# Optimization experiments

Hardware: AMD Instinct MI355X
Metric: run time of the kernel (lower is better)

## Reference

```python
import jax, jax.numpy as jnp
import numpy as np

N = 400_000
E = 3_200_000
K = 5
H = 100
F_IN = 2
L = 5
BN_EPS = 1e-5


def setup_inputs() -> dict:
    key = jax.random.key(0)
    ks = jax.random.split(key, 6)
    x = jax.random.normal(ks[0], (N, F_IN), dtype=jnp.float32)
    edge_index = jax.random.randint(ks[1], (2, E), 0, N, dtype=jnp.int64)
    W0 = jax.random.normal(ks[2], (K, F_IN, H), dtype=jnp.float32) * 0.1
    b0 = jnp.zeros((H,), dtype=jnp.float32)
    Wr = jax.random.normal(ks[3], (L - 1, K, H, H), dtype=jnp.float32) * 0.1
    br = jnp.zeros((L - 1, H), dtype=jnp.float32)
    gamma = jnp.ones((L, H), dtype=jnp.float32)
    beta = jnp.zeros((L, H), dtype=jnp.float32)
    return {"x": x, "edge_index": edge_index, "W0": W0, "b0": b0,
            "Wr": Wr, "br": br, "gamma": gamma, "beta": beta}


def reference(x, edge_index, W0, b0, Wr, br, gamma, beta):
    n = x.shape[0]
    src, dst = edge_index[0], edge_index[1]

    # ChebConv normalization (lambda_max = 2, sym): L_hat = -D^{-1/2} A D^{-1/2}
    deg = jax.ops.segment_sum(jnp.ones(src.shape, jnp.float32), src, num_segments=n)
    dinv = jnp.where(deg > 0, jax.lax.rsqrt(jnp.maximum(deg, 1.0)), 0.0)
    norm = -dinv[src] * dinv[dst]  # [E]

    def prop(h):
        # out[i] = sum_{(j->i)} norm_e * h[j]
        return jax.ops.segment_sum(norm[:, None] * h[src], dst, num_segments=n)

    def cheb(h, W, b):
        # Chebyshev recurrence: T0 = h, T1 = L_hat h, Tk = 2 L_hat T_{k-1} - T_{k-2}
        Tx0 = h
        out = Tx0 @ W[0] + b
        Tx1 = prop(Tx0)
        out = out + Tx1 @ W[1]
        for k in range(2, W.shape[0]):
            Tx2 = 2.0 * prop(Tx1) - Tx0
            out = out + Tx2 @ W[k]
            Tx0, Tx1 = Tx1, Tx2
        return out

    def batch_norm(h, g, bt):
        m = h.mean(axis=0)
        v = h.var(axis=0)  # biased, as torch BN uses for normalization
        return g * (h - m) * jax.lax.rsqrt(v + BN_EPS) + bt

    h = x
    for layer in range(L):
        W = W0 if layer == 0 else Wr[layer - 1]
        b = b0 if layer == 0 else br[layer - 1]
        h = batch_norm(jax.nn.relu(cheb(h, W, b)), gamma[layer], beta[layer])
    return h
```

## Files before the change

### kernel.cpp

```cpp
#include <hip/hip_runtime.h>

#define H 100
#define FIN 2
#define KORD 5
#define NPB 64
#define SE_CAP 2048

typedef unsigned int uint32;
typedef unsigned short ushort16;
typedef __attribute__((ext_vector_type(8))) short s8v;
typedef __attribute__((ext_vector_type(4))) float f4v;

__device__ __forceinline__ ushort16 f2b(float x) {
  uint32 u = __float_as_uint(x);
  return (ushort16)((u + 0x7fffu + ((u >> 16) & 1u)) >> 16);
}
__device__ __forceinline__ float2 b2f2(uint32 v) {
  return make_float2(__uint_as_float(v << 16), __uint_as_float(v & 0xffff0000u));
}
__device__ __forceinline__ void acc8(float* a, uint4 v, float w) {
  float2 f;
  f = b2f2(v.x); a[0] = fmaf(w, f.x, a[0]); a[1] = fmaf(w, f.y, a[1]);
  f = b2f2(v.y); a[2] = fmaf(w, f.x, a[2]); a[3] = fmaf(w, f.y, a[3]);
  f = b2f2(v.z); a[4] = fmaf(w, f.x, a[4]); a[5] = fmaf(w, f.y, a[5]);
  f = b2f2(v.w); a[6] = fmaf(w, f.x, a[6]); a[7] = fmaf(w, f.y, a[7]);
}


__global__ __launch_bounds__(256) void deg_kernel(const int* __restrict__ src, const int* __restrict__ dst,
                                                  float* __restrict__ deg, int* __restrict__ indeg, int E) {
  int e = blockIdx.x * 256 + threadIdx.x;
  if (e < E) {
    atomicAdd(&deg[src[e]], 1.0f);
    atomicAdd(&indeg[dst[e]], 1);
  }
}

__global__ __launch_bounds__(256) void dinv_kernel(const float* __restrict__ deg, float* __restrict__ dinv, int n) {
  int i = blockIdx.x * 256 + threadIdx.x;
  if (i < n) {
    float d = deg[i];
    dinv[i] = d > 0.f ? rsqrtf(fmaxf(d, 1.f)) : 0.f;
  }
}

__global__ __launch_bounds__(256) void scan_block(const int* __restrict__ in, int* __restrict__ incl,
                                                  int* __restrict__ bsum, int n) {
  __shared__ int s[256];
  int i = blockIdx.x * 256 + threadIdx.x;
  int v = (i < n) ? in[i] : 0;
  s[threadIdx.x] = v;
  __syncthreads();
  for (int d = 1; d < 256; d <<= 1) {
    int t = (threadIdx.x >= d) ? s[threadIdx.x - d] : 0;
    __syncthreads();
    s[threadIdx.x] += t;
    __syncthreads();
  }
  if (i < n) incl[i] = s[threadIdx.x];
  if (threadIdx.x == 255) bsum[blockIdx.x] = s[255];
}

__global__ __launch_bounds__(256) void scan_sums(const int* __restrict__ bsum, int* __restrict__ bscan, int nb) {
  __shared__ int s[256];
  __shared__ int carry;
  if (threadIdx.x == 0) carry = 0;
  __syncthreads();
  for (int base = 0; base < nb; base += 256) {
    int i = base + threadIdx.x;
    int v = (i < nb) ? bsum[i] : 0;
    s[threadIdx.x] = v;
    __syncthreads();
    for (int d = 1; d < 256; d <<= 1) {
      int t = (threadIdx.x >= d) ? s[threadIdx.x - d] : 0;
      __syncthreads();
      s[threadIdx.x] += t;
      __syncthreads();
    }
    int c = carry;
    if (i < nb) bscan[i] = s[threadIdx.x] + c;
    __syncthreads();
    if (threadIdx.x == 0) carry = c + s[255];
    __syncthreads();
  }
}

__global__ __launch_bounds__(256) void finalize_offsets(const int* __restrict__ incl, const int* __restrict__ indeg,
                                                        const int* __restrict__ bscan, int* __restrict__ offsets,
                                                        int* __restrict__ cursor, int n, int total) {
  int i = blockIdx.x * 256 + threadIdx.x;
  if (i < n) {
    int prev = (blockIdx.x > 0) ? bscan[blockIdx.x - 1] : 0;
    int excl = incl[i] - indeg[i] + prev;
    offsets[i] = excl;
    cursor[i] = excl;
  }
  if (i == 0) offsets[n] = total;
}

__global__ __launch_bounds__(256) void build_csr(const int* __restrict__ src, const int* __restrict__ dst,
                                                 const float* __restrict__ dinv, int* __restrict__ cursor,
                                                 int2* __restrict__ csr, int E) {
  int e = blockIdx.x * 256 + threadIdx.x;
  if (e < E) {
    int s = src[e], d = dst[e];
    float nrm = -dinv[s] * dinv[d];
    int p = atomicAdd(&cursor[d], 1);
    csr[p] = make_int2(s, __float_as_int(nrm));
  }
}

__global__ __launch_bounds__(256) void pad_zero(uint4* __restrict__ b, int nrows) {
  int i = blockIdx.x * 256 + threadIdx.x;
  if (i < nrows * 4) {
    uint4 z; z.x = 0; z.y = 0; z.z = 0; z.w = 0;
    b[(size_t)(i >> 2) * 16 + 12 + (i & 3)] = z;
  }
}


__global__ __launch_bounds__(256) void prop2(const float* __restrict__ h, const float* __restrict__ prev,
                                             float* __restrict__ out, const int* __restrict__ offs,
                                             const int2* __restrict__ csr, int n, int mode) {
  int i = blockIdx.x * 256 + threadIdx.x;
  if (i >= n) return;
  float a0 = 0.f, a1 = 0.f;
  int e0 = offs[i], e1 = offs[i + 1];
  int e = e0;
  for (; e + 4 <= e1; e += 4) {
    int2 c0 = csr[e], c1 = csr[e + 1], c2 = csr[e + 2], c3 = csr[e + 3];
    float w0 = __int_as_float(c0.y), w1 = __int_as_float(c1.y);
    float w2 = __int_as_float(c2.y), w3 = __int_as_float(c3.y);
    float x0 = h[2 * c0.x], y0 = h[2 * c0.x + 1];
    float x1 = h[2 * c1.x], y1 = h[2 * c1.x + 1];
    float x2 = h[2 * c2.x], y2 = h[2 * c2.x + 1];
    float x3 = h[2 * c3.x], y3 = h[2 * c3.x + 1];
    a0 = fmaf(w0, x0, a0); a1 = fmaf(w0, y0, a1);
    a0 = fmaf(w1, x1, a0); a1 = fmaf(w1, y1, a1);
    a0 = fmaf(w2, x2, a0); a1 = fmaf(w2, y2, a1);
    a0 = fmaf(w3, x3, a0); a1 = fmaf(w3, y3, a1);
  }
  for (; e < e1; ++e) {
    int2 c = csr[e];
    float w = __int_as_float(c.y);
    a0 = fmaf(w, h[2 * c.x], a0);
    a1 = fmaf(w, h[2 * c.x + 1], a1);
  }
  if (mode) {
    a0 = 2.f * a0 - prev[2 * i];
    a1 = 2.f * a1 - prev[2 * i + 1];
  }
  out[2 * i] = a0;
  out[2 * i + 1] = a1;
}

__global__ __launch_bounds__(256) void prop_hb3(const uint32* __restrict__ h, const uint32* __restrict__ prev,
                                                uint32* __restrict__ out, const int* __restrict__ offs,
                                                const int2* __restrict__ csr, int n, int mode) {
  __shared__ int2 se[SE_CAP];
  __shared__ int soff[NPB + 1];
  int t = threadIdx.x;
  int n0 = blockIdx.x * NPB;
  if (t <= NPB) {
    int idx = n0 + t;
    soff[t] = offs[idx < n ? idx : n];
  }
  __syncthreads();
  int e0b = soff[0], e1b = soff[NPB];
  bool staged = (e1b - e0b) <= SE_CAP;
  if (staged) {
    for (int i = e0b + t; i < e1b; i += 256) se[i - e0b] = csr[i];
  }
  __syncthreads();

  int w = t >> 6, lane = t & 63, grp = lane >> 4, sub = lane & 15;
  const uint4* hq = (const uint4*)h;
  uint4* oq = (uint4*)out;
  bool wr = (grp == 0);
  int base = w * 16;
  int cnt = 16;
  if (n0 + base + 16 > n) cnt = n - (n0 + base);
  if (cnt <= 0) return;

  auto nrOf = [&](int li) {
    int d = soff[base + li + 1] - soff[base + li];
    int r = (d + 7) >> 3;
    return r ? r : 1;
  };
  auto issueLoads = [&](int li, int r, uint4& v0, uint4& v1, float& w0, float& w1) {
    int e0 = soff[base + li];
    int deg = soff[base + li + 1] - e0;
    int ea = 8 * r + grp;
    int2 ca = make_int2(0, 0), cb = make_int2(0, 0);
    if (staged) {
      int eb = e0 - e0b;
      if (ea < deg) ca = se[eb + ea];
      if (ea + 4 < deg) cb = se[eb + ea + 4];
    } else {
      if (ea < deg) ca = csr[e0 + ea];
      if (ea + 4 < deg) cb = csr[e0 + ea + 4];
    }
    v0 = hq[(size_t)ca.x * 16 + sub];
    v1 = hq[(size_t)cb.x * 16 + sub];
    w0 = __int_as_float(ca.y);
    w1 = __int_as_float(cb.y);
  };
  auto finishNode = [&](int li, float* a) {
    int node = n0 + base + li;
    size_t qi = (size_t)node * 16 + sub;
    uint4 pv; pv.x = 0; pv.y = 0; pv.z = 0; pv.w = 0;
    if (mode && wr && sub < 13) pv = ((const uint4*)prev)[qi];
#pragma unroll
    for (int j = 0; j < 8; ++j) a[j] += __shfl_xor(a[j], 16);
#pragma unroll
    for (int j = 0; j < 8; ++j) a[j] += __shfl_xor(a[j], 32);
    if (!wr) return;
    if (sub >= 13) {
      uint4 z; z.x = 0; z.y = 0; z.z = 0; z.w = 0;
      oq[qi] = z;
      return;
    }
    if (sub == 12) { a[4] = 0.f; a[5] = 0.f; a[6] = 0.f; a[7] = 0.f; }
    float rr[8];
    if (mode) {
      float2 p;
      p = b2f2(pv.x); rr[0] = 2.f * a[0] - p.x; rr[1] = 2.f * a[1] - p.y;
      p = b2f2(pv.y); rr[2] = 2.f * a[2] - p.x; rr[3] = 2.f * a[3] - p.y;
      p = b2f2(pv.z); rr[4] = 2.f * a[4] - p.x; rr[5] = 2.f * a[5] - p.y;
      p = b2f2(pv.w); rr[6] = 2.f * a[6] - p.x; rr[7] = 2.f * a[7] - p.y;
    } else {
#pragma unroll
      for (int j = 0; j < 8; ++j) rr[j] = a[j];
    }
    uint4 pk;
    pk.x = (uint32)f2b(rr[0]) | ((uint32)f2b(rr[1]) << 16);
    pk.y = (uint32)f2b(rr[2]) | ((uint32)f2b(rr[3]) << 16);
    pk.z = (uint32)f2b(rr[4]) | ((uint32)f2b(rr[5]) << 16);
    pk.w = (uint32)f2b(rr[6]) | ((uint32)f2b(rr[7]) << 16);
    oq[qi] = pk;
  };

  float a[8];
#pragma unroll
  for (int j = 0; j < 8; ++j) a[j] = 0.f;
  int li = 0, r = 0, nr = nrOf(0);
  uint4 va, vb;
  float wa, wb;
  issueLoads(0, 0, va, vb, wa, wb);
  for (;;) {
    int nli = li, nrr = r + 1;
    bool fin = (nrr >= nr);
    if (fin) { nli = li + 1; nrr = 0; }
    bool more = (nli < cnt);
    uint4 va2, vb2;
    float wa2 = 0.f, wb2 = 0.f;
    if (more) issueLoads(nli, nrr, va2, vb2, wa2, wb2);
    acc8(a, va, wa);
    acc8(a, vb, wb);
    if (fin) {
      finishNode(li, a);
#pragma unroll
      for (int j = 0; j < 8; ++j) a[j] = 0.f;
      if (more) nr = nrOf(nli);
    }
    if (!more) break;
    li = nli; r = nrr;
    va = va2; vb = vb2; wa = wa2; wb = wb2;
  }
}


__global__ __launch_bounds__(64) void wconv(const float* __restrict__ Wr, ushort16* __restrict__ Wf) {
  int b = blockIdx.x;
  int l = threadIdx.x;
  int mat = b / 28, rem = b % 28;
  int kc = rem / 7, ft = rem % 7;
  const float* Wm = Wr + (size_t)mat * H * H;
  int c0 = kc * 32 + (l >> 4) * 8;
  int f = ft * 16 + (l & 15);
  ushort16 vals[8];
#pragma unroll
  for (int j = 0; j < 8; ++j) {
    int c = c0 + j;
    float v = (c < H && f < H) ? Wm[c * H + f] : 0.f;
    vals[j] = f2b(v);
  }
  uint4 pk;
  pk.x = (uint32)vals[0] | ((uint32)vals[1] << 16);
  pk.y = (uint32)vals[2] | ((uint32)vals[3] << 16);
  pk.z = (uint32)vals[4] | ((uint32)vals[5] << 16);
  pk.w = (uint32)vals[6] | ((uint32)vals[7] << 16);
  *(uint4*)(Wf + (size_t)b * 512 + l * 8) = pk;
}


__global__ __launch_bounds__(256) void gemm_mfma(const ushort16* __restrict__ Ta, const ushort16* __restrict__ Tb,
                                                 const ushort16* __restrict__ Tc, const ushort16* __restrict__ Td,
                                                 const ushort16* __restrict__ Te, int nk,
                                                 const ushort16* __restrict__ Wf, const float* __restrict__ bias,
                                                 float* __restrict__ C, int n, int initMode,
                                                 float* __restrict__ stats, int doStats) {
  __shared__ float sred[4][2][112];
  int t = threadIdx.x;
  int w = t >> 6, l = t & 63;
  int ml = l & 15, quad = l >> 4;
  int n0 = blockIdx.x * 128 + 32 * w;

  f4v acc[2][7];
  if (initMode) {
#pragma unroll
    for (int ft = 0; ft < 7; ++ft) {
      int f = ft * 16 + ml;
      float b = (f < H) ? bias[f] : 0.f;
      f4v v = {b, b, b, b};
      acc[0][ft] = v;
      acc[1][ft] = v;
    }
  } else {
#pragma unroll
    for (int s = 0; s < 2; ++s)
#pragma unroll
      for (int ft = 0; ft < 7; ++ft) {
        int f = ft * 16 + ml;
#pragma unroll
        for (int r = 0; r < 4; ++r) {
          int row = n0 + 16 * s + quad * 4 + r;
          acc[s][ft][r] = (f < H && row < n) ? C[(size_t)row * H + f] : 0.f;
        }
      }
  }

  for (int k = 0; k < nk; ++k) {
    const ushort16* T = (k == 0) ? Ta : (k == 1) ? Tb : (k == 2) ? Tc : (k == 3) ? Td : Te;
#pragma unroll
    for (int kc = 0; kc < 4; ++kc) {
      s8v bfrag[7];
      const ushort16* wb = Wf + ((size_t)(k * 4 + kc) * 7) * 512 + l * 8;
#pragma unroll
      for (int ft = 0; ft < 7; ++ft) bfrag[ft] = *(const s8v*)(wb + ft * 512);
#pragma unroll
      for (int s = 0; s < 2; ++s) {
        const ushort16* ap = T + (size_t)(n0 + 16 * s + ml) * 128 + kc * 32 + quad * 8;
        s8v a = *(const s8v*)ap;
#pragma unroll
        for (int ft = 0; ft < 7; ++ft)
          acc[s][ft] = __builtin_amdgcn_mfma_f32_16x16x32_bf16(a, bfrag[ft], acc[s][ft], 0, 0, 0);
      }
    }
  }

#pragma unroll
  for (int s = 0; s < 2; ++s)
#pragma unroll
    for (int ft = 0; ft < 7; ++ft) {
      int f = ft * 16 + ml;
      if (f < H) {
#pragma unroll
        for (int r = 0; r < 4; ++r) {
          int row = n0 + 16 * s + quad * 4 + r;
          if (row < n) C[(size_t)row * H + f] = acc[s][ft][r];
        }
      }
    }

  if (doStats) {
#pragma unroll
    for (int ft = 0; ft < 7; ++ft) {
      float s1 = 0.f, s2 = 0.f;
#pragma unroll
      for (int s = 0; s < 2; ++s)
#pragma unroll
        for (int r = 0; r < 4; ++r) {
          int row = n0 + 16 * s + quad * 4 + r;
          float v = (row < n) ? fmaxf(acc[s][ft][r], 0.f) : 0.f;
          s1 += v;
          s2 = fmaf(v, v, s2);
        }
      s1 += __shfl_xor(s1, 16); s1 += __shfl_xor(s1, 32);
      s2 += __shfl_xor(s2, 16); s2 += __shfl_xor(s2, 32);
      if (quad == 0) {
        sred[w][0][ft * 16 + ml] = s1;
        sred[w][1][ft * 16 + ml] = s2;
      }
    }
    __syncthreads();
    if (t < 112 && t < H) {
      float s1 = sred[0][0][t] + sred[1][0][t] + sred[2][0][t] + sred[3][0][t];
      float s2 = sred[0][1][t] + sred[1][1][t] + sred[2][1][t] + sred[3][1][t];
      atomicAdd(&stats[t], s1);
      atomicAdd(&stats[128 + t], s2);
    }
  }
}


__global__ __launch_bounds__(128) void layer0_out(const float* __restrict__ x, const float* __restrict__ t1,
                                                  const float* __restrict__ t2, const float* __restrict__ t3,
                                                  const float* __restrict__ t4, const float* __restrict__ W0,
                                                  const float* __restrict__ b0, float* __restrict__ C, int n) {
  int f = threadIdx.x;
  bool act = f < H;
  float w[10];
  float b = 0.f;
  if (act) {
#pragma unroll
    for (int j = 0; j < 10; ++j) w[j] = W0[j * H + f];
    b = b0[f];
  }
  int n0 = blockIdx.x * 32;
  int n1 = n0 + 32 < n ? n0 + 32 : n;
  for (int i = n0; i < n1; ++i) {
    if (!act) continue;
    float acc = b;
    acc = fmaf(x[2 * i],      w[0], acc);
    acc = fmaf(x[2 * i + 1],  w[1], acc);
    acc = fmaf(t1[2 * i],     w[2], acc);
    acc = fmaf(t1[2 * i + 1], w[3], acc);
    acc = fmaf(t2[2 * i],     w[4], acc);
    acc = fmaf(t2[2 * i + 1], w[5], acc);
    acc = fmaf(t3[2 * i],     w[6], acc);
    acc = fmaf(t3[2 * i + 1], w[7], acc);
    acc = fmaf(t4[2 * i],     w[8], acc);
    acc = fmaf(t4[2 * i + 1], w[9], acc);
    C[(size_t)i * H + f] = acc;
  }
}


__global__ __launch_bounds__(128) void bn_stats(const float* __restrict__ acc, float* __restrict__ stats, int n) {
  int f = threadIdx.x;
  int n0 = blockIdx.x * 512;
  int n1 = n0 + 512 < n ? n0 + 512 : n;
  if (f < H) {
    float s = 0.f, s2 = 0.f;
    for (int i = n0; i < n1; ++i) {
      float v = fmaxf(acc[(size_t)i * H + f], 0.f);
      s += v;
      s2 = fmaf(v, v, s2);
    }
    atomicAdd(&stats[f], s);
    atomicAdd(&stats[128 + f], s2);
  }
}

__global__ __launch_bounds__(128) void bn_params(float* __restrict__ stats, const float* __restrict__ gamma,
                                                 const float* __restrict__ beta, int n) {
  int f = threadIdx.x;
  if (f >= H) return;
  float inv_n = 1.f / (float)n;
  float m = stats[f] * inv_n;
  float v = stats[128 + f] * inv_n - m * m;
  float is = rsqrtf(v + 1e-5f);
  float g = gamma[f] * is;
  stats[256 + f] = g;
  stats[384 + f] = beta[f] - m * g;
}

__global__ __launch_bounds__(256) void bn_final(const float* __restrict__ acc, const float* __restrict__ mi,
                                                float* __restrict__ out, int total) {
  int idx = blockIdx.x * 256 + threadIdx.x;
  if (idx >= total) return;
  int f = idx % H;
  float v = fmaxf(acc[idx], 0.f);
  out[idx] = fmaf(v, mi[f], mi[128 + f]);
}

__global__ __launch_bounds__(256) void bn_final_bf16v(const float* __restrict__ acc, const float* __restrict__ mi,
                                                      uint4* __restrict__ out, int n) {
  int idx = blockIdx.x * 256 + threadIdx.x;
  if (idx >= n * 13) return;
  int row = idx / 13, s = idx - row * 13;
  int f0 = s * 8;
  const float* cr = acc + (size_t)row * H;
  float v[8];
#pragma unroll
  for (int j = 0; j < 8; ++j) {
    int f = f0 + j;
    int fc = (f < H) ? f : 0;
    float c = fmaxf(cr[fc], 0.f);
    v[j] = (f < H) ? fmaf(c, mi[f], mi[128 + f]) : 0.f;
  }
  uint4 pk;
  pk.x = (uint32)f2b(v[0]) | ((uint32)f2b(v[1]) << 16);
  pk.y = (uint32)f2b(v[2]) | ((uint32)f2b(v[3]) << 16);
  pk.z = (uint32)f2b(v[4]) | ((uint32)f2b(v[5]) << 16);
  pk.w = (uint32)f2b(v[6]) | ((uint32)f2b(v[7]) << 16);
  out[(size_t)row * 16 + s] = pk;
}


extern "C" void kernel_launch(void* const* d_in, const int* in_sizes, int n_in,
                              void* d_out, int out_size, void* d_ws, size_t ws_size,
                              hipStream_t stream) {
  const float* x     = (const float*)d_in[0];
  const int*   ei    = (const int*)d_in[1];
  const float* W0    = (const float*)d_in[2];
  const float* b0    = (const float*)d_in[3];
  const float* Wr    = (const float*)d_in[4];
  const float* br    = (const float*)d_in[5];
  const float* gamma = (const float*)d_in[6];
  const float* beta  = (const float*)d_in[7];
  float* C = (float*)d_out;

  const int N = in_sizes[0] / FIN;
  const int E = in_sizes[1] / 2;
  const int* src = ei;
  const int* dst = ei + E;

  char* ws = (char*)d_ws;
  size_t off = 0;
  auto alloc = [&](size_t bytes) -> void* {
    void* p = ws + off;
    off = (off + bytes + 255) & ~(size_t)255;
    return p;
  };

  size_t TB = (size_t)N * 128 * sizeof(ushort16);
  ushort16* B0     = (ushort16*)alloc(TB);
  ushort16* B1     = (ushort16*)alloc(TB);
  ushort16* B2     = (ushort16*)alloc(TB);
  ushort16* Wf     = (ushort16*)alloc((size_t)20 * 14336 * sizeof(ushort16));
  float* t1       = (float*)alloc((size_t)N * 2 * 4);
  float* t2       = (float*)alloc((size_t)N * 2 * 4);
  float* t3       = (float*)alloc((size_t)N * 2 * 4);
  float* t4       = (float*)alloc((size_t)N * 2 * 4);
  float* deg      = (float*)alloc((size_t)N * 4);
  int*   indeg    = (int*)alloc((size_t)N * 4);
  float* dinv     = (float*)alloc((size_t)N * 4);
  int*   incl     = (int*)alloc((size_t)N * 4);
  int*   bsum     = (int*)alloc(8192 * 4);
  int*   bscan    = (int*)alloc(8192 * 4);
  int*   offsets  = (int*)alloc((size_t)(N + 1) * 4);
  int*   cursor   = (int*)alloc((size_t)N * 4);
  int2*  csr      = (int2*)alloc((size_t)E * 8);
  float* stats    = (float*)alloc(512 * 4);

  ushort16* B3 = B0;
  ushort16* B4 = B1;
  bool five = (off + 2 * TB + 512 <= ws_size);
  if (five) {
    B3 = (ushort16*)alloc(TB);
    B4 = (ushort16*)alloc(TB);
  }

  int gE = (E + 255) / 256;
  int gN = (N + 255) / 256;

  hipMemsetAsync(deg, 0, (size_t)N * 4, stream);
  hipMemsetAsync(indeg, 0, (size_t)N * 4, stream);

  deg_kernel<<<gE, 256, 0, stream>>>(src, dst, deg, indeg, E);
  dinv_kernel<<<gN, 256, 0, stream>>>(deg, dinv, N);
  scan_block<<<gN, 256, 0, stream>>>(indeg, incl, bsum, N);
  scan_sums<<<1, 256, 0, stream>>>(bsum, bscan, gN);
  finalize_offsets<<<gN, 256, 0, stream>>>(incl, indeg, bscan, offsets, cursor, N, E);
  build_csr<<<gE, 256, 0, stream>>>(src, dst, dinv, cursor, csr, E);
  wconv<<<20 * 28, 64, 0, stream>>>(Wr, Wf);
  pad_zero<<<(N * 4 + 255) / 256, 256, 0, stream>>>((uint4*)B0, N);

  prop2<<<gN, 256, 0, stream>>>(x,  x,  t1, offsets, csr, N, 0);
  prop2<<<gN, 256, 0, stream>>>(t1, x,  t2, offsets, csr, N, 1);
  prop2<<<gN, 256, 0, stream>>>(t2, t1, t3, offsets, csr, N, 1);
  prop2<<<gN, 256, 0, stream>>>(t3, t2, t4, offsets, csr, N, 1);
  layer0_out<<<(N + 31) / 32, 128, 0, stream>>>(x, t1, t2, t3, t4, W0, b0, C, N);
  hipMemsetAsync(stats, 0, 1024, stream);
  bn_stats<<<(N + 511) / 512, 128, 0, stream>>>(C, stats, N);
  bn_params<<<1, 128, 0, stream>>>(stats, gamma, beta, N);
  bn_final_bf16v<<<(N * 13 + 255) / 256, 256, 0, stream>>>(C, stats + 256, (uint4*)B0, N);

  int gG = (N + 127) / 128;
  int gP = (N + NPB - 1) / NPB;
  for (int layer = 1; layer < 5; ++layer) {
    const ushort16* WfL = Wf + (size_t)(layer - 1) * 5 * 14336;
    const float* bl = br + (size_t)(layer - 1) * H;
    if (five) {
      prop_hb3<<<gP, 256, 0, stream>>>((const uint32*)B0, (const uint32*)B0, (uint32*)B1, offsets, csr, N, 0);
      prop_hb3<<<gP, 256, 0, stream>>>((const uint32*)B1, (const uint32*)B0, (uint32*)B2, offsets, csr, N, 1);
      prop_hb3<<<gP, 256, 0, stream>>>((const uint32*)B2, (const uint32*)B1, (uint32*)B3, offsets, csr, N, 1);
      prop_hb3<<<gP, 256, 0, stream>>>((const uint32*)B3, (const uint32*)B2, (uint32*)B4, offsets, csr, N, 1);
      hipMemsetAsync(stats, 0, 1024, stream);
      gemm_mfma<<<gG, 256, 0, stream>>>(B0, B1, B2, B3, B4, 5, WfL, bl, C, N, 1, stats, 1);
    } else {
      prop_hb3<<<gP, 256, 0, stream>>>((const uint32*)B0, (const uint32*)B0, (uint32*)B1, offsets, csr, N, 0);
      prop_hb3<<<gP, 256, 0, stream>>>((const uint32*)B1, (const uint32*)B0, (uint32*)B2, offsets, csr, N, 1);
      gemm_mfma<<<gG, 256, 0, stream>>>(B0, B1, B2, B0, B1, 3, WfL, bl, C, N, 1, stats, 0);
      prop_hb3<<<gP, 256, 0, stream>>>((const uint32*)B2, (const uint32*)B1, (uint32*)B0, offsets, csr, N, 1);
      prop_hb3<<<gP, 256, 0, stream>>>((const uint32*)B0, (const uint32*)B2, (uint32*)B1, offsets, csr, N, 1);
      gemm_mfma<<<gG, 256, 0, stream>>>(B0, B1, B0, B0, B1, 2, WfL + (size_t)3 * 14336, bl, C, N, 0, stats, 0);
      hipMemsetAsync(stats, 0, 1024, stream);
      bn_stats<<<(N + 511) / 512, 128, 0, stream>>>(C, stats, N);
    }
    bn_params<<<1, 128, 0, stream>>>(stats, gamma + (size_t)layer * H, beta + (size_t)layer * H, N);
    if (layer < 4)
      bn_final_bf16v<<<(N * 13 + 255) / 256, 256, 0, stream>>>(C, stats + 256, (uint4*)B0, N);
    else
      bn_final<<<(N * H + 255) / 256, 256, 0, stream>>>(C, stats + 256, C, N * H);
  }
}
```

Baseline: 4.915 ms.

## Split bf16 feature buffers into 96-wide main and 4-wide tail arrays

Measured after the change: 5.239 ms. +6.6%, slower.

```diff
diff --git a/kernel.cpp b/kernel.cpp
--- a/kernel.cpp
+++ b/kernel.cpp
@@ -107,14 +107,6 @@
     float nrm = -dinv[s] * dinv[d];
     int p = atomicAdd(&cursor[d], 1);
     csr[p] = make_int2(s, __float_as_int(nrm));
-  }
-}
-
-__global__ __launch_bounds__(256) void pad_zero(uint4* __restrict__ b, int nrows) {
-  int i = blockIdx.x * 256 + threadIdx.x;
-  if (i < nrows * 4) {
-    uint4 z; z.x = 0; z.y = 0; z.z = 0; z.w = 0;
-    b[(size_t)(i >> 2) * 16 + 12 + (i & 3)] = z;
   }
 }
 
@@ -154,9 +146,11 @@
   out[2 * i + 1] = a1;
 }
 
-__global__ __launch_bounds__(256) void prop_hb3(const uint32* __restrict__ h, const uint32* __restrict__ prev,
-                                                uint32* __restrict__ out, const int* __restrict__ offs,
-                                                const int2* __restrict__ csr, int n, int mode) {
+__global__ __launch_bounds__(256) void prop_hs(const uint4* __restrict__ mIn, const uint2* __restrict__ tIn,
+                                               const uint4* __restrict__ mPrev, const uint2* __restrict__ tPrev,
+                                               uint4* __restrict__ mOut, uint2* __restrict__ tOut,
+                                               const int* __restrict__ offs, const int2* __restrict__ csr,
+                                               int n, int mode) {
   __shared__ int2 se[SE_CAP];
   __shared__ int soff[NPB + 1];
   int t = threadIdx.x;
@@ -174,8 +168,6 @@
   __syncthreads();
 
   int w = t >> 6, lane = t & 63, grp = lane >> 4, sub = lane & 15;
-  const uint4* hq = (const uint4*)h;
-  uint4* oq = (uint4*)out;
   bool wr = (grp == 0);
   int base = w * 16;
   int cnt = 16;
@@ -200,27 +192,31 @@
       if (ea < deg) ca = csr[e0 + ea];
       if (ea + 4 < deg) cb = csr[e0 + ea + 4];
     }
-    v0 = hq[(size_t)ca.x * 16 + sub];
-    v1 = hq[(size_t)cb.x * 16 + sub];
+    uint4 z; z.x = 0; z.y = 0; z.z = 0; z.w = 0;
+    v0 = z; v1 = z;
+    if (sub < 12) {
+      v0 = mIn[(size_t)ca.x * 12 + sub];
+      v1 = mIn[(size_t)cb.x * 12 + sub];
+    } else if (sub == 12) {
+      uint2 ta = tIn[ca.x], tb = tIn[cb.x];
+      v0.x = ta.x; v0.y = ta.y;
+      v1.x = tb.x; v1.y = tb.y;
+    }
     w0 = __int_as_float(ca.y);
     w1 = __int_as_float(cb.y);
   };
   auto finishNode = [&](int li, float* a) {
     int node = n0 + base + li;
-    size_t qi = (size_t)node * 16 + sub;
     uint4 pv; pv.x = 0; pv.y = 0; pv.z = 0; pv.w = 0;
-    if (mode && wr && sub < 13) pv = ((const uint4*)prev)[qi];
+    if (mode && wr) {
+      if (sub < 12) pv = mPrev[(size_t)node * 12 + sub];
+      else if (sub == 12) { uint2 tp = tPrev[node]; pv.x = tp.x; pv.y = tp.y; }
+    }
 #pragma unroll
     for (int j = 0; j < 8; ++j) a[j] += __shfl_xor(a[j], 16);
 #pragma unroll
     for (int j = 0; j < 8; ++j) a[j] += __shfl_xor(a[j], 32);
-    if (!wr) return;
-    if (sub >= 13) {
-      uint4 z; z.x = 0; z.y = 0; z.z = 0; z.w = 0;
-      oq[qi] = z;
-      return;
-    }
-    if (sub == 12) { a[4] = 0.f; a[5] = 0.f; a[6] = 0.f; a[7] = 0.f; }
+    if (!wr || sub > 12) return;
     float rr[8];
     if (mode) {
       float2 p;
@@ -232,12 +228,19 @@
 #pragma unroll
       for (int j = 0; j < 8; ++j) rr[j] = a[j];
     }
-    uint4 pk;
-    pk.x = (uint32)f2b(rr[0]) | ((uint32)f2b(rr[1]) << 16);
-    pk.y = (uint32)f2b(rr[2]) | ((uint32)f2b(rr[3]) << 16);
-    pk.z = (uint32)f2b(rr[4]) | ((uint32)f2b(rr[5]) << 16);
-    pk.w = (uint32)f2b(rr[6]) | ((uint32)f2b(rr[7]) << 16);
-    oq[qi] = pk;
+    if (sub < 12) {
+      uint4 pk;
+      pk.x = (uint32)f2b(rr[0]) | ((uint32)f2b(rr[1]) << 16);
+      pk.y = (uint32)f2b(rr[2]) | ((uint32)f2b(rr[3]) << 16);
+      pk.z = (uint32)f2b(rr[4]) | ((uint32)f2b(rr[5]) << 16);
+      pk.w = (uint32)f2b(rr[6]) | ((uint32)f2b(rr[7]) << 16);
+      mOut[(size_t)node * 12 + sub] = pk;
+    } else {
+      uint2 pk;
+      pk.x = (uint32)f2b(rr[0]) | ((uint32)f2b(rr[1]) << 16);
+      pk.y = (uint32)f2b(rr[2]) | ((uint32)f2b(rr[3]) << 16);
+      tOut[node] = pk;
+    }
   };
 
   float a[8];
@@ -294,44 +297,33 @@
 }
 
 
-__global__ __launch_bounds__(256) void gemm_mfma(const ushort16* __restrict__ Ta, const ushort16* __restrict__ Tb,
-                                                 const ushort16* __restrict__ Tc, const ushort16* __restrict__ Td,
-                                                 const ushort16* __restrict__ Te, int nk,
+__global__ __launch_bounds__(256) void gemm_mfma(const ushort16* __restrict__ m0, const uint2* __restrict__ t0,
+                                                 const ushort16* __restrict__ m1, const uint2* __restrict__ t1,
+                                                 const ushort16* __restrict__ m2, const uint2* __restrict__ t2,
+                                                 const ushort16* __restrict__ m3, const uint2* __restrict__ t3,
+                                                 const ushort16* __restrict__ m4, const uint2* __restrict__ t4,
                                                  const ushort16* __restrict__ Wf, const float* __restrict__ bias,
-                                                 float* __restrict__ C, int n, int initMode,
-                                                 float* __restrict__ stats, int doStats) {
+                                                 float* __restrict__ C, int n, float* __restrict__ stats) {
   __shared__ float sred[4][2][112];
-  int t = threadIdx.x;
-  int w = t >> 6, l = t & 63;
+  int tid = threadIdx.x;
+  int w = tid >> 6, l = tid & 63;
   int ml = l & 15, quad = l >> 4;
   int n0 = blockIdx.x * 128 + 32 * w;
 
   f4v acc[2][7];
-  if (initMode) {
-#pragma unroll
-    for (int ft = 0; ft < 7; ++ft) {
-      int f = ft * 16 + ml;
-      float b = (f < H) ? bias[f] : 0.f;
-      f4v v = {b, b, b, b};
-      acc[0][ft] = v;
-      acc[1][ft] = v;
-    }
-  } else {
-#pragma unroll
-    for (int s = 0; s < 2; ++s)
-#pragma unroll
-      for (int ft = 0; ft < 7; ++ft) {
-        int f = ft * 16 + ml;
-#pragma unroll
-        for (int r = 0; r < 4; ++r) {
-          int row = n0 + 16 * s + quad * 4 + r;
-          acc[s][ft][r] = (f < H && row < n) ? C[(size_t)row * H + f] : 0.f;
-        }
-      }
-  }
-
-  for (int k = 0; k < nk; ++k) {
-    const ushort16* T = (k == 0) ? Ta : (k == 1) ? Tb : (k == 2) ? Tc : (k == 3) ? Td : Te;
+#pragma unroll
+  for (int ft = 0; ft < 7; ++ft) {
+    int f = ft * 16 + ml;
+    float b = (f < H) ? bias[f] : 0.f;
+    f4v v = {b, b, b, b};
+    acc[0][ft] = v;
+    acc[1][ft] = v;
+  }
+
+#pragma unroll
+  for (int k = 0; k < 5; ++k) {
+    const ushort16* Tm = (k == 0) ? m0 : (k == 1) ? m1 : (k == 2) ? m2 : (k == 3) ? m3 : m4;
+    const uint2* Tt = (k == 0) ? t0 : (k == 1) ? t1 : (k == 2) ? t2 : (k == 3) ? t3 : t4;
 #pragma unroll
     for (int kc = 0; kc < 4; ++kc) {
       s8v bfrag[7];
@@ -340,8 +332,19 @@
       for (int ft = 0; ft < 7; ++ft) bfrag[ft] = *(const s8v*)(wb + ft * 512);
 #pragma unroll
       for (int s = 0; s < 2; ++s) {
-        const ushort16* ap = T + (size_t)(n0 + 16 * s + ml) * 128 + kc * 32 + quad * 8;
-        s8v a = *(const s8v*)ap;
+        int row = n0 + 16 * s + ml;
+        s8v a;
+        if (kc < 3) {
+          a = *(const s8v*)(Tm + (size_t)row * 96 + kc * 32 + quad * 8);
+        } else {
+          s8v az = {0, 0, 0, 0, 0, 0, 0, 0};
+          if (quad == 0) {
+            uint2 tv = Tt[row];
+            az[0] = (short)(tv.x & 0xffffu); az[1] = (short)(tv.x >> 16);
+            az[2] = (short)(tv.y & 0xffffu); az[3] = (short)(tv.y >> 16);
+          }
+          a = az;
+        }
 #pragma unroll
         for (int ft = 0; ft < 7; ++ft)
           acc[s][ft] = __builtin_amdgcn_mfma_f32_16x16x32_bf16(a, bfrag[ft], acc[s][ft], 0, 0, 0);
@@ -363,33 +366,31 @@
       }
     }
 
-  if (doStats) {
-#pragma unroll
-    for (int ft = 0; ft < 7; ++ft) {
-      float s1 = 0.f, s2 = 0.f;
-#pragma unroll
-      for (int s = 0; s < 2; ++s)
-#pragma unroll
-        for (int r = 0; r < 4; ++r) {
-          int row = n0 + 16 * s + quad * 4 + r;
-          float v = (row < n) ? fmaxf(acc[s][ft][r], 0.f) : 0.f;
-          s1 += v;
-          s2 = fmaf(v, v, s2);
-        }
-      s1 += __shfl_xor(s1, 16); s1 += __shfl_xor(s1, 32);
-      s2 += __shfl_xor(s2, 16); s2 += __shfl_xor(s2, 32);
-      if (quad == 0) {
-        sred[w][0][ft * 16 + ml] = s1;
-        sred[w][1][ft * 16 + ml] = s2;
+#pragma unroll
+  for (int ft = 0; ft < 7; ++ft) {
+    float s1 = 0.f, s2 = 0.f;
+#pragma unroll
+    for (int s = 0; s < 2; ++s)
+#pragma unroll
+      for (int r = 0; r < 4; ++r) {
+        int row = n0 + 16 * s + quad * 4 + r;
+        float v = (row < n) ? fmaxf(acc[s][ft][r], 0.f) : 0.f;
+        s1 += v;
+        s2 = fmaf(v, v, s2);
       }
-    }
-    __syncthreads();
-    if (t < 112 && t < H) {
-      float s1 = sred[0][0][t] + sred[1][0][t] + sred[2][0][t] + sred[3][0][t];
-      float s2 = sred[0][1][t] + sred[1][1][t] + sred[2][1][t] + sred[3][1][t];
-      atomicAdd(&stats[t], s1);
-      atomicAdd(&stats[128 + t], s2);
-    }
+    s1 += __shfl_xor(s1, 16); s1 += __shfl_xor(s1, 32);
+    s2 += __shfl_xor(s2, 16); s2 += __shfl_xor(s2, 32);
+    if (quad == 0) {
+      sred[w][0][ft * 16 + ml] = s1;
+      sred[w][1][ft * 16 + ml] = s2;
+    }
+  }
+  __syncthreads();
+  if (tid < H) {
+    float s1 = sred[0][0][tid] + sred[1][0][tid] + sred[2][0][tid] + sred[3][0][tid];
+    float s2 = sred[0][1][tid] + sred[1][1][tid] + sred[2][1][tid] + sred[3][1][tid];
+    atomicAdd(&stats[tid], s1);
+    atomicAdd(&stats[128 + tid], s2);
   }
 }
 
@@ -465,27 +466,40 @@
   out[idx] = fmaf(v, mi[f], mi[128 + f]);
 }
 
-__global__ __launch_bounds__(256) void bn_final_bf16v(const float* __restrict__ acc, const float* __restrict__ mi,
-                                                      uint4* __restrict__ out, int n) {
+__global__ __launch_bounds__(256) void bn_final_split(const float* __restrict__ acc, const float* __restrict__ mi,
+                                                      uint4* __restrict__ mOut, uint2* __restrict__ tOut, int n) {
   int idx = blockIdx.x * 256 + threadIdx.x;
   if (idx >= n * 13) return;
   int row = idx / 13, s = idx - row * 13;
-  int f0 = s * 8;
   const float* cr = acc + (size_t)row * H;
-  float v[8];
-#pragma unroll
-  for (int j = 0; j < 8; ++j) {
-    int f = f0 + j;
-    int fc = (f < H) ? f : 0;
-    float c = fmaxf(cr[fc], 0.f);
-    v[j] = (f < H) ? fmaf(c, mi[f], mi[128 + f]) : 0.f;
-  }
-  uint4 pk;
-  pk.x = (uint32)f2b(v[0]) | ((uint32)f2b(v[1]) << 16);
-  pk.y = (uint32)f2b(v[2]) | ((uint32)f2b(v[3]) << 16);
-  pk.z = (uint32)f2b(v[4]) | ((uint32)f2b(v[5]) << 16);
-  pk.w = (uint32)f2b(v[6]) | ((uint32)f2b(v[7]) << 16);
-  out[(size_t)row * 16 + s] = pk;
+  if (s < 12) {
+    int f0 = s * 8;
+    float v[8];
+#pragma unroll
+    for (int j = 0; j < 8; ++j) {
+      int f = f0 + j;
+      float c = fmaxf(cr[f], 0.f);
+      v[j] = fmaf(c, mi[f], mi[128 + f]);
+    }
+    uint4 pk;
+    pk.x = (uint32)f2b(v[0]) | ((uint32)f2b(v[1]) << 16);
+    pk.y = (uint32)f2b(v[2]) | ((uint32)f2b(v[3]) << 16);
+    pk.z = (uint32)f2b(v[4]) | ((uint32)f2b(v[5]) << 16);
+    pk.w = (uint32)f2b(v[6]) | ((uint32)f2b(v[7]) << 16);
+    mOut[(size_t)row * 12 + s] = pk;
+  } else {
+    float v[4];
+#pragma unroll
+    for (int j = 0; j < 4; ++j) {
+      int f = 96 + j;
+      float c = fmaxf(cr[f], 0.f);
+      v[j] = fmaf(c, mi[f], mi[128 + f]);
+    }
+    uint2 pk;
+    pk.x = (uint32)f2b(v[0]) | ((uint32)f2b(v[1]) << 16);
+    pk.y = (uint32)f2b(v[2]) | ((uint32)f2b(v[3]) << 16);
+    tOut[row] = pk;
+  }
 }
 
 
@@ -515,33 +529,27 @@
     return p;
   };
 
-  size_t TB = (size_t)N * 128 * sizeof(ushort16);
-  ushort16* B0     = (ushort16*)alloc(TB);
-  ushort16* B1     = (ushort16*)alloc(TB);
-  ushort16* B2     = (ushort16*)alloc(TB);
-  ushort16* Wf     = (ushort16*)alloc((size_t)20 * 14336 * sizeof(ushort16));
-  float* t1       = (float*)alloc((size_t)N * 2 * 4);
-  float* t2       = (float*)alloc((size_t)N * 2 * 4);
-  float* t3       = (float*)alloc((size_t)N * 2 * 4);
-  float* t4       = (float*)alloc((size_t)N * 2 * 4);
-  float* deg      = (float*)alloc((size_t)N * 4);
-  int*   indeg    = (int*)alloc((size_t)N * 4);
-  float* dinv     = (float*)alloc((size_t)N * 4);
-  int*   incl     = (int*)alloc((size_t)N * 4);
-  int*   bsum     = (int*)alloc(8192 * 4);
-  int*   bscan    = (int*)alloc(8192 * 4);
-  int*   offsets  = (int*)alloc((size_t)(N + 1) * 4);
-  int*   cursor   = (int*)alloc((size_t)N * 4);
-  int2*  csr      = (int2*)alloc((size_t)E * 8);
-  float* stats    = (float*)alloc(512 * 4);
-
-  ushort16* B3 = B0;
-  ushort16* B4 = B1;
-  bool five = (off + 2 * TB + 512 <= ws_size);
-  if (five) {
-    B3 = (ushort16*)alloc(TB);
-    B4 = (ushort16*)alloc(TB);
-  }
+  size_t MBsz = (size_t)N * 96 * 2;
+  size_t TBsz = (size_t)N * 8;
+  ushort16* Bm[5];
+  uint2*    Bt[5];
+  for (int i = 0; i < 5; ++i) Bm[i] = (ushort16*)alloc(MBsz);
+  for (int i = 0; i < 5; ++i) Bt[i] = (uint2*)alloc(TBsz);
+  ushort16* Wf   = (ushort16*)alloc((size_t)20 * 14336 * sizeof(ushort16));
+  float* t1      = (float*)alloc((size_t)N * 2 * 4);
+  float* t2      = (float*)alloc((size_t)N * 2 * 4);
+  float* t3      = (float*)alloc((size_t)N * 2 * 4);
+  float* t4      = (float*)alloc((size_t)N * 2 * 4);
+  float* deg     = (float*)alloc((size_t)N * 4);
+  int*   indeg   = (int*)alloc((size_t)N * 4);
+  float* dinv    = (float*)alloc((size_t)N * 4);
+  int*   incl    = (int*)alloc((size_t)N * 4);
+  int*   bsum    = (int*)alloc(8192 * 4);
+  int*   bscan   = (int*)alloc(8192 * 4);
+  int*   offsets = (int*)alloc((size_t)(N + 1) * 4);
+  int*   cursor  = (int*)alloc((size_t)N * 4);
+  int2*  csr     = (int2*)alloc((size_t)E * 8);
+  float* stats   = (float*)alloc(512 * 4);
 
   int gE = (E + 255) / 256;
   int gN = (N + 255) / 256;
@@ -556,7 +564,6 @@
   finalize_offsets<<<gN, 256, 0, stream>>>(incl, indeg, bscan, offsets, cursor, N, E);
   build_csr<<<gE, 256, 0, stream>>>(src, dst, dinv, cursor, csr, E);
   wconv<<<20 * 28, 64, 0, stream>>>(Wr, Wf);
-  pad_zero<<<(N * 4 + 255) / 256, 256, 0, stream>>>((uint4*)B0, N);
 
   prop2<<<gN, 256, 0, stream>>>(x,  x,  t1, offsets, csr, N, 0);
   prop2<<<gN, 256, 0, stream>>>(t1, x,  t2, offsets, csr, N, 1);
@@ -566,33 +573,27 @@
   hipMemsetAsync(stats, 0, 1024, stream);
   bn_stats<<<(N + 511) / 512, 128, 0, stream>>>(C, stats, N);
   bn_params<<<1, 128, 0, stream>>>(stats, gamma, beta, N);
-  bn_final_bf16v<<<(N * 13 + 255) / 256, 256, 0, stream>>>(C, stats + 256, (uint4*)B0, N);
+  bn_final_split<<<(N * 13 + 255) / 256, 256, 0, stream>>>(C, stats + 256, (uint4*)Bm[0], Bt[0], N);
 
   int gG = (N + 127) / 128;
   int gP = (N + NPB - 1) / NPB;
   for (int layer = 1; layer < 5; ++layer) {
     const ushort16* WfL = Wf + (size_t)(layer - 1) * 5 * 14336;
     const float* bl = br + (size_t)(layer - 1) * H;
-    if (five) {
-      prop_hb3<<<gP, 256, 0, stream>>>((const uint32*)B0, (const uint32*)B0, (uint32*)B1, offsets, csr, N, 0);
-      prop_hb3<<<gP, 256, 0, stream>>>((const uint32*)B1, (const uint32*)B0, (uint32*)B2, offsets, csr, N, 1);
-      prop_hb3<<<gP, 256, 0, stream>>>((const uint32*)B2, (const uint32*)B1, (uint32*)B3, offsets, csr, N, 1);
-      prop_hb3<<<gP, 256, 0, stream>>>((const uint32*)B3, (const uint32*)B2, (uint32*)B4, offsets, csr, N, 1);
-      hipMemsetAsync(stats, 0, 1024, stream);
-      gemm_mfma<<<gG, 256, 0, stream>>>(B0, B1, B2, B3, B4, 5, WfL, bl, C, N, 1, stats, 1);
-    } else {
-      prop_hb3<<<gP, 256, 0, stream>>>((const uint32*)B0, (const uint32*)B0, (uint32*)B1, offsets, csr, N, 0);
-      prop_hb3<<<gP, 256, 0, stream>>>((const uint32*)B1, (const uint32*)B0, (uint32*)B2, offsets, csr, N, 1);
-      gemm_mfma<<<gG, 256, 0, stream>>>(B0, B1, B2, B0, B1, 3, WfL, bl, C, N, 1, stats, 0);
-      prop_hb3<<<gP, 256, 0, stream>>>((const uint32*)B2, (const uint32*)B1, (uint32*)B0, offsets, csr, N, 1);
-      prop_hb3<<<gP, 256, 0, stream>>>((const uint32*)B0, (const uint32*)B2, (uint32*)B1, offsets, csr, N, 1);
-      gemm_mfma<<<gG, 256, 0, stream>>>(B0, B1, B0, B0, B1, 2, WfL + (size_t)3 * 14336, bl, C, N, 0, stats, 0);
-      hipMemsetAsync(stats, 0, 1024, stream);
-      bn_stats<<<(N + 511) / 512, 128, 0, stream>>>(C, stats, N);
-    }
+    prop_hs<<<gP, 256, 0, stream>>>((const uint4*)Bm[0], Bt[0], (const uint4*)Bm[0], Bt[0],
+                                    (uint4*)Bm[1], Bt[1], offsets, csr, N, 0);
+    prop_hs<<<gP, 256, 0, stream>>>((const uint4*)Bm[1], Bt[1], (const uint4*)Bm[0], Bt[0],
+                                    (uint4*)Bm[2], Bt[2], offsets, csr, N, 1);
+    prop_hs<<<gP, 256, 0, stream>>>((const uint4*)Bm[2], Bt[2], (const uint4*)Bm[1], Bt[1],
+                                    (uint4*)Bm[3], Bt[3], offsets, csr, N, 1);
+    prop_hs<<<gP, 256, 0, stream>>>((const uint4*)Bm[3], Bt[3], (const uint4*)Bm[2], Bt[2],
+                                    (uint4*)Bm[4], Bt[4], offsets, csr, N, 1);
+    hipMemsetAsync(stats, 0, 1024, stream);
+    gemm_mfma<<<gG, 256, 0, stream>>>(Bm[0], Bt[0], Bm[1], Bt[1], Bm[2], Bt[2], Bm[3], Bt[3], Bm[4], Bt[4],
+                                      WfL, bl, C, N, stats);
     bn_params<<<1, 128, 0, stream>>>(stats, gamma + (size_t)layer * H, beta + (size_t)layer * H, N);
     if (layer < 4)
-      bn_final_bf16v<<<(N * 13 + 255) / 256, 256, 0, stream>>>(C, stats + 256, (uint4*)B0, N);
+      bn_final_split<<<(N * 13 + 255) / 256, 256, 0, stream>>>(C, stats + 256, (uint4*)Bm[0], Bt[0], N);
     else
       bn_final<<<(N * H + 255) / 256, 256, 0, stream>>>(C, stats + 256, C, N * H);
   }
```
